# Kernel optimization log

Measured on AMD Instinct MI355X. Metric: run time of the kernel, lower is better.

The kernel has to match this reference:

```python
import jax, jax.numpy as jnp
import numpy as np

NUM_HEADS = 16
HIDDEN = 1024
HEAD_DIM = HIDDEN // NUM_HEADS
B, L = 2, 2048


def setup_inputs() -> dict:
    key = jax.random.key(0)
    ks = jax.random.split(key, 5)
    scale = 1.0 / np.sqrt(HIDDEN)
    return {
        "x": jax.random.normal(ks[0], (B, L, HIDDEN), dtype=jnp.float32),
        "Wq": jax.random.normal(ks[1], (HIDDEN, HIDDEN), dtype=jnp.float32) * scale,
        "Wk": jax.random.normal(ks[2], (HIDDEN, HIDDEN), dtype=jnp.float32) * scale,
        "Wv": jax.random.normal(ks[3], (HIDDEN, HIDDEN), dtype=jnp.float32) * scale,
        "Wo": jax.random.normal(ks[4], (HIDDEN, HIDDEN), dtype=jnp.float32) * scale,
    }


def reference(x, Wq, Wk, Wv, Wo):
    b, l, _ = x.shape
    # projections (torch nn.Linear: y = x @ W.T), reshape to (B,L,H,D)
    q = (x @ Wq.T).reshape(b, l, NUM_HEADS, HEAD_DIM)
    k = (x @ Wk.T).reshape(b, l, NUM_HEADS, HEAD_DIM)
    v = (x @ Wv.T).reshape(b, l, NUM_HEADS, HEAD_DIM)
    # positive feature map
    q = jax.nn.elu(q) + 1.0
    k = jax.nn.elu(k) + 1.0
    # causal linear attention via cumulative kv outer products
    kv = jnp.einsum('blhd,blhe->blhde', k, v)          # (B,L,H,D,D)
    kv_cumsum = jnp.cumsum(kv, axis=1)
    k_cumsum = jnp.cumsum(k, axis=1)
    out = jnp.einsum('blhd,blhde->blhe', q, kv_cumsum)  # (B,L,H,D)
    normalizer = jnp.clip(jnp.einsum('blhd,blhd->blh', q, k_cumsum), 1e-6, None)
    out = out / normalizer[..., None]
    out = out.reshape(b, l, HIDDEN)
    return out @ Wo.T
```

## Files before the change

kernel.cpp:

```cpp
#include <hip/hip_runtime.h>
#include <cstdint>
#include <cstddef>

#define HID 1024
#define NH 16
#define HD 64
#define BB 2
#define LL 2048
#define MM (BB*LL)
#define CHUNK 64
#define NT (LL/CHUNK)
#define NSEG 16
#define BHn (BB*NH)
#define SP 72

typedef __bf16 bf16;
typedef __attribute__((ext_vector_type(8))) __bf16 bf16x8;
typedef __attribute__((ext_vector_type(4))) float f32x4;

__device__ __forceinline__ f32x4 mfma16(bf16x8 a, bf16x8 b, f32x4 c){
  return __builtin_amdgcn_mfma_f32_16x16x32_bf16(a, b, c, 0, 0, 0);
}

__device__ __forceinline__ void gload16(const void* g, void* l){
  __builtin_amdgcn_global_load_lds(
      (const __attribute__((address_space(1))) unsigned int*)g,
      (__attribute__((address_space(3))) unsigned int*)l, 16, 0, 0);
}

__device__ __forceinline__ void barx(){
  asm volatile("" ::: "memory");
  __builtin_amdgcn_s_barrier();
  asm volatile("" ::: "memory");
}

#define WAITVM(N) asm volatile("s_waitcnt vmcnt(" #N ")" ::: "memory")

__global__ __launch_bounds__(256) void cast_all_k(
    const float* __restrict__ x,  const float* __restrict__ w0,
    const float* __restrict__ w1, const float* __restrict__ w2, const float* __restrict__ w3,
    bf16* __restrict__ xb, bf16* __restrict__ d0, bf16* __restrict__ d1,
    bf16* __restrict__ d2, bf16* __restrict__ d3)
{
  int bid = blockIdx.x;
  const float* s; bf16* d; int base;
  if (bid < 2048){ s = x; d = xb; base = bid; }
  else {
    int w = (bid - 2048) >> 9, r = (bid - 2048) & 511;
    s = (w==0)?w0:(w==1)?w1:(w==2)?w2:w3;
    d = (w==0)?d0:(w==1)?d1:(w==2)?d2:d3;
    base = r;
  }
  size_t i = (size_t)(base*256 + threadIdx.x) * 8;
  float4 v0 = *(const float4*)(s + i);
  float4 v1 = *(const float4*)(s + i + 4);
  union { bf16 h[8]; uint4 u; } pk;
  pk.h[0]=(bf16)v0.x; pk.h[1]=(bf16)v0.y; pk.h[2]=(bf16)v0.z; pk.h[3]=(bf16)v0.w;
  pk.h[4]=(bf16)v1.x; pk.h[5]=(bf16)v1.y; pk.h[6]=(bf16)v1.z; pk.h[7]=(bf16)v1.w;
  *(uint4*)(d + i) = pk.u;
}

template<int MODE>
__global__ __launch_bounds__(512, 2) void gemm8_k(
    const bf16* __restrict__ A,
    const bf16* __restrict__ W0, const bf16* __restrict__ W1, const bf16* __restrict__ W2,
    bf16* __restrict__ Qo, bf16* __restrict__ Kn, bf16* __restrict__ Vn,
    float* __restrict__ Outf)
{
  constexpr int NKT = HID/32;
  __shared__ bf16 lds[4][2][128*32];

  const int tid = threadIdx.x;
  const int wv = tid >> 6, lane = tid & 63;
  const int lrow = lane & 15, g4 = lane >> 4;
  const int wr = wv >> 2, wc = wv & 3;
  int bn = blockIdx.x, wsel = 0;
  const bf16* W = W0;
  if (MODE==0){ wsel = bn >> 3; bn &= 7; W = (wsel==0)?W0:((wsel==1)?W1:W2); }
  const int row0 = blockIdx.y*128, col0 = bn*128;

  const int sr = tid >> 2, sc = tid & 3;
  const int scs = sc ^ ((sr>>1)&3);
  const bf16* gA = A + (size_t)(row0 + sr)*HID + scs*8;
  const bf16* gB = W + (size_t)(col0 + sr)*HID + scs*8;
  const int ldst = tid*8;

  auto stage_tile = [&](int u){
    const int buf = u & 3;
    gload16(gA + u*32, (void*)&lds[buf][0][ldst]);
    gload16(gB + u*32, (void*)&lds[buf][1][ldst]);
  };

  const int koff = (g4 ^ ((lrow>>1)&3)) << 3;

  auto read_frags = [&](int u, bf16x8 (&fa)[4], bf16x8 (&fb)[2]){
    const int buf = u & 3;
    #pragma unroll
    for (int i=0;i<4;i++)
      fa[i] = *(const bf16x8*)&lds[buf][0][((wr*64 + i*16+lrow)<<5) + koff];
    #pragma unroll
    for (int j=0;j<2;j++)
      fb[j] = *(const bf16x8*)&lds[buf][1][((wc*32 + j*16+lrow)<<5) + koff];
  };

  f32x4 acc[4][2] = {};
  auto do_mfma = [&](bf16x8 (&fa)[4], bf16x8 (&fb)[2]){
    __builtin_amdgcn_s_setprio(1);
    #pragma unroll
    for (int i=0;i<4;i++)
      #pragma unroll
      for (int j=0;j<2;j++)
        acc[i][j] = mfma16(fa[i], fb[j], acc[i][j]);
    __builtin_amdgcn_s_setprio(0);
  };

  stage_tile(0); stage_tile(1); stage_tile(2);
  WAITVM(4);
  barx();
  bf16x8 fEa[4], fEb[2], fOa[4], fOb[2];
  read_frags(0, fEa, fEb);

  for (int t=0; t<NKT; t+=2){
    if (t+3 < NKT)      { stage_tile(t+3); WAITVM(4); }
    else if (t+3 == NKT){ WAITVM(2); }
    else                { WAITVM(0); }
    barx();
    read_frags(t+1, fOa, fOb);
    do_mfma(fEa, fEb);
    const int t2 = t+1;
    if (t2 < NKT-1){
      if (t2+3 < NKT)      { stage_tile(t2+3); WAITVM(4); }
      else if (t2+3 == NKT){ WAITVM(2); }
      else                 { WAITVM(0); }
      barx();
      read_frags(t2+1, fEa, fEb);
    }
    do_mfma(fOa, fOb);
  }

  #pragma unroll
  for (int i=0;i<4;i++){
    const int m0 = row0 + wr*64 + i*16 + g4*4;
    #pragma unroll
    for (int j=0;j<2;j++){
      const int c = col0 + wc*32 + j*16 + lrow;
      #pragma unroll
      for (int r=0;r<4;r++){
        float v = acc[i][j][r];
        if (MODE==1){
          Outf[(size_t)(m0+r)*HID + c] = v;
        } else {
          if (wsel<2) v = v>0.f ? v+1.f : __expf(v);
          bf16 bv = (bf16)v;
          if      (wsel==0) Qo[(size_t)(m0+r)*HID + c] = bv;
          else if (wsel==1) Kn[(size_t)(m0+r)*HID + c] = bv;
          else              Vn[(size_t)(m0+r)*HID + c] = bv;
        }
      }
    }
  }
}

__global__ __launch_bounds__(256, 2) void segsum_k(const bf16* __restrict__ Kn, const bf16* __restrict__ Vn,
                                                   float* __restrict__ Sseg, float* __restrict__ kseg)
{
  __shared__ bf16 KT[64*SP];
  __shared__ bf16 VT[64*SP];
  const int bx = blockIdx.x;
  const int bh = bx >> 4, seg = bx & (NSEG-1);
  const int b = bh>>4, h = bh&15;
  const int tid = threadIdx.x;
  const int we = tid >> 6, lane = tid & 63;
  const int lrow = lane&15, g4 = lane>>4, lk8 = g4*8;
  const int sj = tid >> 2, c4 = tid & 3;

  f32x4 acc[4] = {};
  float krow = 0.f;

  #pragma unroll
  for (int c=0;c<2;c++){
    const int cg = seg*2 + c;
    const bf16* kb = Kn + ((size_t)(b*LL + cg*CHUNK))*HID + h*HD;
    const bf16* vb = Vn + ((size_t)(b*LL + cg*CHUNK))*HID + h*HD;
    {
      const bf16* ks = kb + (size_t)sj*HID + c4*16;
      const bf16* vs = vb + (size_t)sj*HID + c4*16;
      bf16x8 kr0 = *(const bf16x8*)&ks[0], kr1 = *(const bf16x8*)&ks[8];
      bf16x8 vr0 = *(const bf16x8*)&vs[0], vr1 = *(const bf16x8*)&vs[8];
      #pragma unroll
      for (int e=0;e<8;e++){
        KT[(c4*16+e)*SP + sj]   = kr0[e];
        KT[(c4*16+8+e)*SP + sj] = kr1[e];
        VT[(c4*16+e)*SP + sj]   = vr0[e];
        VT[(c4*16+8+e)*SP + sj] = vr1[e];
      }
    }
    __syncthreads();
    #pragma unroll
    for (int kk=0;kk<2;kk++){
      bf16x8 fa = *(const bf16x8*)&VT[(we*16 + lrow)*SP + kk*32 + lk8];
      #pragma unroll
      for (int j=0;j<4;j++){
        bf16x8 fb = *(const bf16x8*)&KT[(j*16 + lrow)*SP + kk*32 + lk8];
        acc[j] = mfma16(fa, fb, acc[j]);
      }
    }
    {
      const int row = we*16 + lrow;
      float s = 0.f;
      #pragma unroll
      for (int u=0;u<2;u++){
        bf16x8 k8 = *(const bf16x8*)&KT[row*SP + g4*16 + u*8];
        #pragma unroll
        for (int e=0;e<8;e++) s += (float)k8[e];
      }
      s += __shfl_xor(s,16); s += __shfl_xor(s,32);
      krow += s;
    }
    __syncthreads();
  }

  float* so = Sseg + (size_t)bx*4096;
  #pragma unroll
  for (int j=0;j<4;j++)
    #pragma unroll
    for (int r=0;r<4;r++)
      so[(we*16 + g4*4 + r)*64 + j*16 + lrow] = acc[j][r];
  if (g4==0) kseg[(size_t)bx*64 + we*16 + lrow] = krow;
}

__global__ __launch_bounds__(256) void segscan_k(const float* __restrict__ Sseg, const float* __restrict__ kseg,
                                                 bf16* __restrict__ Sexb, float* __restrict__ ksxb)
{
  int gid = blockIdx.x*256 + threadIdx.x;
  if (gid < BHn*4096){
    int bh = gid >> 12, e = gid & 4095;
    float run = 0.f;
    size_t base = (size_t)bh*NSEG*4096 + e;
    #pragma unroll 4
    for (int s=0;s<NSEG;s++){
      Sexb[base + (size_t)s*4096] = (bf16)run;
      run += Sseg[base + (size_t)s*4096];
    }
  } else if (gid < BHn*4096 + BHn*64){
    int g2 = gid - BHn*4096;
    int bh = g2 >> 6, d = g2 & 63;
    float run = 0.f;
    size_t base = (size_t)bh*NSEG*64 + d;
    #pragma unroll 4
    for (int s=0;s<NSEG;s++){
      ksxb[base + (size_t)s*64] = run;
      run += kseg[base + (size_t)s*64];
    }
  }
}

__global__ __launch_bounds__(256, 2) void attn_k(const bf16* __restrict__ Q, const bf16* __restrict__ Kn,
                                                 const bf16* __restrict__ Vn, const bf16* __restrict__ Sexb,
                                                 const float* __restrict__ ksxb, bf16* __restrict__ Obuf)
{
  __shared__ bf16 KT[64*SP];
  __shared__ bf16 VT[64*SP];
  __shared__ bf16 P [64*SP];
  __shared__ bf16 Sm[64*SP];
  __shared__ float ksum_lds[64];
  const int bx = blockIdx.x;
  const int bh = bx >> 4, seg = bx & (NSEG-1);
  const int b = bh>>4, h = bh&15;
  const int tid = threadIdx.x;
  const int w = tid >> 6, lane = tid & 63;
  const int lrow = lane&15, g4 = lane>>4, lk8 = g4*8;
  const int sj = tid >> 2, c4 = tid & 3;

  if (tid < 64) ksum_lds[tid] = ksxb[(size_t)bx*64 + tid];
  {
    const bf16* sp = Sexb + (size_t)bx*4096 + tid*16;
    bf16x8 s0 = *(const bf16x8*)&sp[0], s1 = *(const bf16x8*)&sp[8];
    const int e = tid>>2, d0 = (tid&3)*16;
    *(bf16x8*)&Sm[e*SP + d0]     = s0;
    *(bf16x8*)&Sm[e*SP + d0 + 8] = s1;
  }
  __syncthreads();
  f32x4 Srun[4];
  #pragma unroll
  for (int j=0;j<4;j++)
    #pragma unroll
    for (int r=0;r<4;r++)
      Srun[j][r] = (float)Sm[(w*16+g4*4+r)*SP + j*16+lrow];

  #pragma unroll
  for (int c=0;c<2;c++){
    const int cg = seg*2 + c;
    const bf16* kb = Kn + ((size_t)(b*LL + cg*CHUNK))*HID + h*HD;
    const bf16* vb = Vn + ((size_t)(b*LL + cg*CHUNK))*HID + h*HD;
    const bf16* qb = Q  + ((size_t)(b*LL + cg*CHUNK))*HID + h*HD;
    {
      const bf16* ks = kb + (size_t)sj*HID + c4*16;
      const bf16* vs = vb + (size_t)sj*HID + c4*16;
      bf16x8 kr0 = *(const bf16x8*)&ks[0], kr1 = *(const bf16x8*)&ks[8];
      bf16x8 vr0 = *(const bf16x8*)&vs[0], vr1 = *(const bf16x8*)&vs[8];
      #pragma unroll
      for (int e=0;e<8;e++){
        KT[(c4*16+e)*SP + sj]   = kr0[e];
        KT[(c4*16+8+e)*SP + sj] = kr1[e];
        VT[(c4*16+e)*SP + sj]   = vr0[e];
        VT[(c4*16+8+e)*SP + sj] = vr1[e];
      }
    }
    bf16x8 aq[2], bk[4][2];
    #pragma unroll
    for (int kk=0;kk<2;kk++){
      aq[kk] = *(const bf16x8*)&qb[(size_t)(w*16+lrow)*HID + kk*32 + lk8];
      #pragma unroll
      for (int j=0;j<4;j++)
        bk[j][kk] = *(const bf16x8*)&kb[(size_t)(j*16+lrow)*HID + kk*32 + lk8];
    }
    __syncthreads();
    f32x4 sacc[4] = {};
    #pragma unroll
    for (int kk=0;kk<2;kk++)
      #pragma unroll
      for (int j=0;j<4;j++)
        sacc[j] = mfma16(aq[kk], bk[j][kk], sacc[j]);
    float rs[4];
    #pragma unroll
    for (int r=0;r<4;r++){
      int irow = w*16 + g4*4 + r;
      float p = 0.f;
      #pragma unroll
      for (int j=0;j<4;j++){
        int jcol = j*16 + lrow;
        float v = (jcol <= irow) ? sacc[j][r] : 0.f;
        sacc[j][r] = v;
        p += v;
      }
      p += __shfl_xor(p,1); p += __shfl_xor(p,2);
      p += __shfl_xor(p,4); p += __shfl_xor(p,8);
      rs[r] = p;
    }
    float zA;
    {
      float s = 0.f;
      #pragma unroll
      for (int kk=0;kk<2;kk++){
        const float* k8 = ksum_lds + kk*32 + lk8;
        bf16x8 q = aq[kk];
        #pragma unroll
        for (int j=0;j<8;j++) s += (float)q[j] * k8[j];
      }
      s += __shfl_xor(s,16); s += __shfl_xor(s,32);
      zA = s;
    }
    f32x4 oacc[4] = {};
    #pragma unroll
    for (int kk=0;kk<2;kk++)
      #pragma unroll
      for (int j=0;j<4;j++){
        bf16x8 bs = *(const bf16x8*)&Sm[(j*16+lrow)*SP + kk*32 + lk8];
        oacc[j] = mfma16(aq[kk], bs, oacc[j]);
      }
    #pragma unroll
    for (int j=0;j<4;j++)
      #pragma unroll
      for (int r=0;r<4;r++)
        P[(w*16+g4*4+r)*SP + j*16+lrow] = (bf16)sacc[j][r];
    __syncthreads();
    #pragma unroll
    for (int kk=0;kk<2;kk++){
      bf16x8 ap = *(const bf16x8*)&P[(w*16+lrow)*SP + kk*32 + lk8];
      #pragma unroll
      for (int j=0;j<4;j++){
        bf16x8 bv = *(const bf16x8*)&VT[(j*16+lrow)*SP + kk*32 + lk8];
        oacc[j] = mfma16(ap, bv, oacc[j]);
      }
    }
    bf16* ob = Obuf + ((size_t)(b*LL + cg*CHUNK))*HID + h*HD;
    #pragma unroll
    for (int r=0;r<4;r++){
      float z = __shfl(zA, g4*4 + r) + rs[r];
      z = fmaxf(z, 1e-6f);
      float inv = 1.0f/z;
      int irow = w*16 + g4*4 + r;
      #pragma unroll
      for (int j=0;j<4;j++)
        ob[(size_t)irow*HID + j*16+lrow] = (bf16)(oacc[j][r]*inv);
    }
    if (c==0){
      #pragma unroll
      for (int kk=0;kk<2;kk++){
        bf16x8 fa = *(const bf16x8*)&VT[(w*16+lrow)*SP + kk*32 + lk8];
        #pragma unroll
        for (int j=0;j<4;j++){
          bf16x8 fb = *(const bf16x8*)&KT[(j*16+lrow)*SP + kk*32 + lk8];
          Srun[j] = mfma16(fa, fb, Srun[j]);
        }
      }
      {
        const int row = w*16 + lrow;
        float s = 0.f;
        #pragma unroll
        for (int u=0;u<2;u++){
          bf16x8 k8 = *(const bf16x8*)&KT[row*SP + g4*16 + u*8];
          #pragma unroll
          for (int e=0;e<8;e++) s += (float)k8[e];
        }
        s += __shfl_xor(s,16); s += __shfl_xor(s,32);
        if (g4==0) ksum_lds[row] += s;
      }
      #pragma unroll
      for (int j=0;j<4;j++)
        #pragma unroll
        for (int r=0;r<4;r++)
          Sm[(w*16+g4*4+r)*SP + j*16+lrow] = (bf16)Srun[j][r];
    }
    __syncthreads();
  }
}

extern "C" void kernel_launch(void* const* d_in, const int* in_sizes, int n_in,
                              void* d_out, int out_size, void* d_ws, size_t ws_size,
                              hipStream_t stream)
{
  const float* x  = (const float*)d_in[0];
  const float* Wq = (const float*)d_in[1];
  const float* Wk = (const float*)d_in[2];
  const float* Wv = (const float*)d_in[3];
  const float* Wo = (const float*)d_in[4];
  float* out = (float*)d_out;

  char* p = (char*)d_ws;
  auto alloc = [&](size_t bytes){ void* r = (void*)p; p += (bytes + 255) & ~(size_t)255; return r; };
  bf16* xb   = (bf16*)alloc((size_t)MM*HID*2);
  bf16* Wqb  = (bf16*)alloc((size_t)HID*HID*2);
  bf16* Wkb  = (bf16*)alloc((size_t)HID*HID*2);
  bf16* Wvb  = (bf16*)alloc((size_t)HID*HID*2);
  bf16* Wob  = (bf16*)alloc((size_t)HID*HID*2);
  bf16* Qb   = (bf16*)alloc((size_t)MM*HID*2);
  bf16* Knb  = (bf16*)alloc((size_t)MM*HID*2);
  bf16* Vnb  = (bf16*)alloc((size_t)MM*HID*2);
  bf16* Ob   = (bf16*)alloc((size_t)MM*HID*2);
  float* Sseg = (float*)alloc((size_t)BHn*NSEG*4096*4);
  bf16*  Sexb = (bf16*) alloc((size_t)BHn*NSEG*4096*2);
  float* kseg = (float*)alloc((size_t)BHn*NSEG*64*4);
  float* ksxb = (float*)alloc((size_t)BHn*NSEG*64*4);

  cast_all_k<<<dim3(4096), 256, 0, stream>>>(x, Wq,Wk,Wv,Wo, xb, Wqb,Wkb,Wvb,Wob);
  gemm8_k<0><<<dim3(24,32), 512, 0, stream>>>(xb, Wqb,Wkb,Wvb, Qb,Knb,Vnb, nullptr);
  segsum_k<<<dim3(BHn*NSEG), 256, 0, stream>>>(Knb, Vnb, Sseg, kseg);
  segscan_k<<<dim3((BHn*4096 + BHn*64 + 255)/256), 256, 0, stream>>>(Sseg, kseg, Sexb, ksxb);
  attn_k<<<dim3(BHn*NSEG), 256, 0, stream>>>(Qb, Knb, Vnb, Sexb, ksxb, Ob);
  gemm8_k<1><<<dim3(8,32), 512, 0, stream>>>(Ob, Wob,nullptr,nullptr, nullptr,nullptr,nullptr, out);
}
```

Baseline: 150.4 us.

## Write transposed K and V from projection GEMM epilogue, drop LDS transposes

The QKV projection epilogue now stages K and V tiles through shared memory and writes them head-major and transposed (d by sequence), alongside the row-major K. The segment-sum and attention kernels then read MFMA fragments directly from global memory instead of doing scattered LDS transposes, which removes per-element LDS stores and one barrier per chunk. The cost is an extra K write, strided global fragment loads, and an added LDS round trip in the GEMM epilogue.

Measured after the change: 161.6 us. 1.07x slower.

```diff
diff --git a/kernel.cpp b/kernel.cpp
--- a/kernel.cpp
+++ b/kernel.cpp
@@ -9,7 +9,6 @@
 #define LL 2048
 #define MM (BB*LL)
 #define CHUNK 64
-#define NT (LL/CHUNK)
 #define NSEG 16
 #define BHn (BB*NH)
 #define SP 72
@@ -64,8 +63,8 @@
 __global__ __launch_bounds__(512, 2) void gemm8_k(
     const bf16* __restrict__ A,
     const bf16* __restrict__ W0, const bf16* __restrict__ W1, const bf16* __restrict__ W2,
-    bf16* __restrict__ Qo, bf16* __restrict__ Kn, bf16* __restrict__ Vn,
-    float* __restrict__ Outf)
+    bf16* __restrict__ Qo, bf16* __restrict__ Kn, bf16* __restrict__ Kt,
+    bf16* __restrict__ Vt, float* __restrict__ Outf)
 {
   constexpr int NKT = HID/32;
   __shared__ bf16 lds[4][2][128*32];
@@ -138,95 +137,106 @@
     do_mfma(fOa, fOb);
   }
 
-  #pragma unroll
-  for (int i=0;i<4;i++){
-    const int m0 = row0 + wr*64 + i*16 + g4*4;
-    #pragma unroll
-    for (int j=0;j<2;j++){
-      const int c = col0 + wc*32 + j*16 + lrow;
-      #pragma unroll
-      for (int r=0;r<4;r++){
-        float v = acc[i][j][r];
-        if (MODE==1){
-          Outf[(size_t)(m0+r)*HID + c] = v;
-        } else {
-          if (wsel<2) v = v>0.f ? v+1.f : __expf(v);
+  if (MODE==1){
+    #pragma unroll
+    for (int i=0;i<4;i++){
+      const int m0 = row0 + wr*64 + i*16 + g4*4;
+      #pragma unroll
+      for (int j=0;j<2;j++){
+        const int c = col0 + wc*32 + j*16 + lrow;
+        #pragma unroll
+        for (int r=0;r<4;r++)
+          Outf[(size_t)(m0+r)*HID + c] = acc[i][j][r];
+      }
+    }
+  } else if (wsel==0){
+    #pragma unroll
+    for (int i=0;i<4;i++){
+      const int m0 = row0 + wr*64 + i*16 + g4*4;
+      #pragma unroll
+      for (int j=0;j<2;j++){
+        const int c = col0 + wc*32 + j*16 + lrow;
+        #pragma unroll
+        for (int r=0;r<4;r++){
+          float v = acc[i][j][r];
+          v = v>0.f ? v+1.f : __expf(v);
+          Qo[(size_t)(m0+r)*HID + c] = (bf16)v;
+        }
+      }
+    }
+  } else {
+    bf16* T = &lds[0][0][0];
+    barx();
+    #pragma unroll
+    for (int i=0;i<4;i++){
+      const int ml0 = wr*64 + i*16 + g4*4;
+      const int m0  = row0 + ml0;
+      #pragma unroll
+      for (int j=0;j<2;j++){
+        const int cc = wc*32 + j*16 + lrow;
+        #pragma unroll
+        for (int r=0;r<4;r++){
+          float v = acc[i][j][r];
+          if (wsel==1) v = v>0.f ? v+1.f : __expf(v);
           bf16 bv = (bf16)v;
-          if      (wsel==0) Qo[(size_t)(m0+r)*HID + c] = bv;
-          else if (wsel==1) Kn[(size_t)(m0+r)*HID + c] = bv;
-          else              Vn[(size_t)(m0+r)*HID + c] = bv;
+          if (wsel==1) Kn[(size_t)(m0+r)*HID + (col0+cc)] = bv;
+          T[cc*136 + ml0 + r] = bv;
         }
       }
     }
-  }
-}
-
-__global__ __launch_bounds__(256, 2) void segsum_k(const bf16* __restrict__ Kn, const bf16* __restrict__ Vn,
-                                                   float* __restrict__ Sseg, float* __restrict__ kseg)
-{
-  __shared__ bf16 KT[64*SP];
-  __shared__ bf16 VT[64*SP];
+    barx();
+    bf16* dst = (wsel==1) ? Kt : Vt;
+    const int cc = tid >> 2, mlb = (tid & 3) * 32;
+    const int cgl = col0 + cc;
+    const int hh = cgl >> 6, dd = cgl & 63;
+    const int bseq = row0 >> 11, lbase = (row0 & (LL-1)) + mlb;
+    size_t base = ((size_t)((bseq*NH + hh)*HD + dd))*LL + lbase;
+    #pragma unroll
+    for (int u=0;u<4;u++)
+      *(bf16x8*)&dst[base + u*8] = *(const bf16x8*)&T[cc*136 + mlb + u*8];
+  }
+}
+
+__global__ __launch_bounds__(256) void segsum_k(const bf16* __restrict__ Kt, const bf16* __restrict__ Vt,
+                                                float* __restrict__ Sseg, float* __restrict__ kseg)
+{
   const int bx = blockIdx.x;
   const int bh = bx >> 4, seg = bx & (NSEG-1);
-  const int b = bh>>4, h = bh&15;
   const int tid = threadIdx.x;
   const int we = tid >> 6, lane = tid & 63;
   const int lrow = lane&15, g4 = lane>>4, lk8 = g4*8;
-  const int sj = tid >> 2, c4 = tid & 3;
+  const bf16* ktb = Kt + (size_t)bh*HD*LL + seg*128;
+  const bf16* vtb = Vt + (size_t)bh*HD*LL + seg*128;
 
   f32x4 acc[4] = {};
-  float krow = 0.f;
-
   #pragma unroll
-  for (int c=0;c<2;c++){
-    const int cg = seg*2 + c;
-    const bf16* kb = Kn + ((size_t)(b*LL + cg*CHUNK))*HID + h*HD;
-    const bf16* vb = Vn + ((size_t)(b*LL + cg*CHUNK))*HID + h*HD;
-    {
-      const bf16* ks = kb + (size_t)sj*HID + c4*16;
-      const bf16* vs = vb + (size_t)sj*HID + c4*16;
-      bf16x8 kr0 = *(const bf16x8*)&ks[0], kr1 = *(const bf16x8*)&ks[8];
-      bf16x8 vr0 = *(const bf16x8*)&vs[0], vr1 = *(const bf16x8*)&vs[8];
-      #pragma unroll
-      for (int e=0;e<8;e++){
-        KT[(c4*16+e)*SP + sj]   = kr0[e];
-        KT[(c4*16+8+e)*SP + sj] = kr1[e];
-        VT[(c4*16+e)*SP + sj]   = vr0[e];
-        VT[(c4*16+8+e)*SP + sj] = vr1[e];
-      }
-    }
-    __syncthreads();
-    #pragma unroll
-    for (int kk=0;kk<2;kk++){
-      bf16x8 fa = *(const bf16x8*)&VT[(we*16 + lrow)*SP + kk*32 + lk8];
-      #pragma unroll
-      for (int j=0;j<4;j++){
-        bf16x8 fb = *(const bf16x8*)&KT[(j*16 + lrow)*SP + kk*32 + lk8];
-        acc[j] = mfma16(fa, fb, acc[j]);
-      }
-    }
-    {
-      const int row = we*16 + lrow;
-      float s = 0.f;
-      #pragma unroll
-      for (int u=0;u<2;u++){
-        bf16x8 k8 = *(const bf16x8*)&KT[row*SP + g4*16 + u*8];
-        #pragma unroll
-        for (int e=0;e<8;e++) s += (float)k8[e];
-      }
-      s += __shfl_xor(s,16); s += __shfl_xor(s,32);
-      krow += s;
-    }
-    __syncthreads();
-  }
-
+  for (int kk=0;kk<4;kk++){
+    bf16x8 fa = *(const bf16x8*)&vtb[(size_t)(we*16+lrow)*LL + kk*32 + lk8];
+    #pragma unroll
+    for (int j=0;j<4;j++){
+      bf16x8 fb = *(const bf16x8*)&ktb[(size_t)(j*16+lrow)*LL + kk*32 + lk8];
+      acc[j] = mfma16(fa, fb, acc[j]);
+    }
+  }
   float* so = Sseg + (size_t)bx*4096;
   #pragma unroll
   for (int j=0;j<4;j++)
     #pragma unroll
     for (int r=0;r<4;r++)
       so[(we*16 + g4*4 + r)*64 + j*16 + lrow] = acc[j][r];
-  if (g4==0) kseg[(size_t)bx*64 + we*16 + lrow] = krow;
+
+  {
+    float s = 0.f;
+    const bf16* kr = ktb + (size_t)(we*16+lrow)*LL + g4*32;
+    #pragma unroll
+    for (int u=0;u<4;u++){
+      bf16x8 k8 = *(const bf16x8*)&kr[u*8];
+      #pragma unroll
+      for (int e=0;e<8;e++) s += (float)k8[e];
+    }
+    s += __shfl_xor(s,16); s += __shfl_xor(s,32);
+    if (g4==0) kseg[(size_t)bx*64 + we*16 + lrow] = s;
+  }
 }
 
 __global__ __launch_bounds__(256) void segscan_k(const float* __restrict__ Sseg, const float* __restrict__ kseg,
@@ -256,11 +266,10 @@
 }
 
 __global__ __launch_bounds__(256, 2) void attn_k(const bf16* __restrict__ Q, const bf16* __restrict__ Kn,
-                                                 const bf16* __restrict__ Vn, const bf16* __restrict__ Sexb,
-                                                 const float* __restrict__ ksxb, bf16* __restrict__ Obuf)
-{
-  __shared__ bf16 KT[64*SP];
-  __shared__ bf16 VT[64*SP];
+                                                 const bf16* __restrict__ Kt, const bf16* __restrict__ Vt,
+                                                 const bf16* __restrict__ Sexb, const float* __restrict__ ksxb,
+                                                 bf16* __restrict__ Obuf)
+{
   __shared__ bf16 P [64*SP];
   __shared__ bf16 Sm[64*SP];
   __shared__ float ksum_lds[64];
@@ -270,7 +279,8 @@
   const int tid = threadIdx.x;
   const int w = tid >> 6, lane = tid & 63;
   const int lrow = lane&15, g4 = lane>>4, lk8 = g4*8;
-  const int sj = tid >> 2, c4 = tid & 3;
+  const bf16* ktb = Kt + (size_t)bh*HD*LL + seg*128;
+  const bf16* vtb = Vt + (size_t)bh*HD*LL + seg*128;
 
   if (tid < 64) ksum_lds[tid] = ksxb[(size_t)bx*64 + tid];
   {
@@ -292,21 +302,7 @@
   for (int c=0;c<2;c++){
     const int cg = seg*2 + c;
     const bf16* kb = Kn + ((size_t)(b*LL + cg*CHUNK))*HID + h*HD;
-    const bf16* vb = Vn + ((size_t)(b*LL + cg*CHUNK))*HID + h*HD;
     const bf16* qb = Q  + ((size_t)(b*LL + cg*CHUNK))*HID + h*HD;
-    {
-      const bf16* ks = kb + (size_t)sj*HID + c4*16;
-      const bf16* vs = vb + (size_t)sj*HID + c4*16;
-      bf16x8 kr0 = *(const bf16x8*)&ks[0], kr1 = *(const bf16x8*)&ks[8];
-      bf16x8 vr0 = *(const bf16x8*)&vs[0], vr1 = *(const bf16x8*)&vs[8];
-      #pragma unroll
-      for (int e=0;e<8;e++){
-        KT[(c4*16+e)*SP + sj]   = kr0[e];
-        KT[(c4*16+8+e)*SP + sj] = kr1[e];
-        VT[(c4*16+e)*SP + sj]   = vr0[e];
-        VT[(c4*16+8+e)*SP + sj] = vr1[e];
-      }
-    }
     bf16x8 aq[2], bk[4][2];
     #pragma unroll
     for (int kk=0;kk<2;kk++){
@@ -315,7 +311,6 @@
       for (int j=0;j<4;j++)
         bk[j][kk] = *(const bf16x8*)&kb[(size_t)(j*16+lrow)*HID + kk*32 + lk8];
     }
-    __syncthreads();
     f32x4 sacc[4] = {};
     #pragma unroll
     for (int kk=0;kk<2;kk++)
@@ -370,7 +365,7 @@
       bf16x8 ap = *(const bf16x8*)&P[(w*16+lrow)*SP + kk*32 + lk8];
       #pragma unroll
       for (int j=0;j<4;j++){
-        bf16x8 bv = *(const bf16x8*)&VT[(j*16+lrow)*SP + kk*32 + lk8];
+        bf16x8 bv = *(const bf16x8*)&vtb[(size_t)(j*16+lrow)*LL + c*64 + kk*32 + lk8];
         oacc[j] = mfma16(ap, bv, oacc[j]);
       }
     }
@@ -388,32 +383,32 @@
     if (c==0){
       #pragma unroll
       for (int kk=0;kk<2;kk++){
-        bf16x8 fa = *(const bf16x8*)&VT[(w*16+lrow)*SP + kk*32 + lk8];
+        bf16x8 fa = *(const bf16x8*)&vtb[(size_t)(w*16+lrow)*LL + kk*32 + lk8];
         #pragma unroll
         for (int j=0;j<4;j++){
-          bf16x8 fb = *(const bf16x8*)&KT[(j*16+lrow)*SP + kk*32 + lk8];
+          bf16x8 fb = *(const bf16x8*)&ktb[(size_t)(j*16+lrow)*LL + kk*32 + lk8];
           Srun[j] = mfma16(fa, fb, Srun[j]);
         }
       }
       {
-        const int row = w*16 + lrow;
         float s = 0.f;
+        const bf16* kr = ktb + (size_t)(w*16+lrow)*LL + g4*16;
         #pragma unroll
         for (int u=0;u<2;u++){
-          bf16x8 k8 = *(const bf16x8*)&KT[row*SP + g4*16 + u*8];
+          bf16x8 k8 = *(const bf16x8*)&kr[u*8];
           #pragma unroll
           for (int e=0;e<8;e++) s += (float)k8[e];
         }
         s += __shfl_xor(s,16); s += __shfl_xor(s,32);
-        if (g4==0) ksum_lds[row] += s;
+        if (g4==0) ksum_lds[w*16+lrow] += s;
       }
       #pragma unroll
       for (int j=0;j<4;j++)
         #pragma unroll
         for (int r=0;r<4;r++)
           Sm[(w*16+g4*4+r)*SP + j*16+lrow] = (bf16)Srun[j][r];
-    }
-    __syncthreads();
+      __syncthreads();
+    }
   }
 }
 
@@ -437,7 +432,8 @@
   bf16* Wob  = (bf16*)alloc((size_t)HID*HID*2);
   bf16* Qb   = (bf16*)alloc((size_t)MM*HID*2);
   bf16* Knb  = (bf16*)alloc((size_t)MM*HID*2);
-  bf16* Vnb  = (bf16*)alloc((size_t)MM*HID*2);
+  bf16* Ktb  = (bf16*)alloc((size_t)MM*HID*2);
+  bf16* Vtb  = (bf16*)alloc((size_t)MM*HID*2);
   bf16* Ob   = (bf16*)alloc((size_t)MM*HID*2);
   float* Sseg = (float*)alloc((size_t)BHn*NSEG*4096*4);
   bf16*  Sexb = (bf16*) alloc((size_t)BHn*NSEG*4096*2);
@@ -445,9 +441,9 @@
   float* ksxb = (float*)alloc((size_t)BHn*NSEG*64*4);
 
   cast_all_k<<<dim3(4096), 256, 0, stream>>>(x, Wq,Wk,Wv,Wo, xb, Wqb,Wkb,Wvb,Wob);
-  gemm8_k<0><<<dim3(24,32), 512, 0, stream>>>(xb, Wqb,Wkb,Wvb, Qb,Knb,Vnb, nullptr);
-  segsum_k<<<dim3(BHn*NSEG), 256, 0, stream>>>(Knb, Vnb, Sseg, kseg);
+  gemm8_k<0><<<dim3(24,32), 512, 0, stream>>>(xb, Wqb,Wkb,Wvb, Qb,Knb,Ktb,Vtb, nullptr);
+  segsum_k<<<dim3(BHn*NSEG), 256, 0, stream>>>(Ktb, Vtb, Sseg, kseg);
   segscan_k<<<dim3((BHn*4096 + BHn*64 + 255)/256), 256, 0, stream>>>(Sseg, kseg, Sexb, ksxb);
-  attn_k<<<dim3(BHn*NSEG), 256, 0, stream>>>(Qb, Knb, Vnb, Sexb, ksxb, Ob);
-  gemm8_k<1><<<dim3(8,32), 512, 0, stream>>>(Ob, Wob,nullptr,nullptr, nullptr,nullptr,nullptr, out);
-}
+  attn_k<<<dim3(BHn*NSEG), 256, 0, stream>>>(Qb, Knb, Ktb, Vtb, Sexb, ksxb, Ob);
+  gemm8_k<1><<<dim3(8,32), 512, 0, stream>>>(Ob, Wob,nullptr,nullptr, nullptr,nullptr,nullptr,nullptr, out);
+}
```
